# Optimization experiments

Measured on AMD Instinct MI355X. Metric: run time of the kernel, lower is better.

Reference implementation:

```python
import jax, jax.numpy as jnp
import numpy as np

N = 50000
E = 800000
IN, HID, OUT = 20, 64, 2
HEADS, HD = 4, 64
EPS = 1e-5


def setup_inputs() -> dict:
    key = jax.random.key(0)
    ks = jax.random.split(key, 24)
    rn = lambda k, shape, s=0.1: (jax.random.normal(k, shape, dtype=jnp.float32) * s)
    inp = {}
    inp['x'] = jax.random.normal(ks[0], (N, IN), dtype=jnp.float32)
    inp['edge_index'] = jax.random.randint(ks[1], (2, E), 0, N, dtype=jnp.int64)
    # SAGEConv1: lin_l (aggregated msgs, bias), lin_r (root, no bias)
    inp['Wl1'] = rn(ks[2], (IN, HID)); inp['Wr1'] = rn(ks[3], (IN, HID)); inp['b1'] = jnp.zeros((HID,), jnp.float32)
    inp['g1'] = jnp.ones((HID,), jnp.float32); inp['bt1'] = jnp.zeros((HID,), jnp.float32)
    # GATConv: W2 projects to heads*dim; att vectors per head; bias size HID (concat=False)
    inp['W2'] = rn(ks[4], (HID, HEADS * HD)); inp['att_src'] = rn(ks[5], (HEADS, HD)); inp['att_dst'] = rn(ks[6], (HEADS, HD)); inp['b2'] = jnp.zeros((HID,), jnp.float32)
    inp['g2'] = jnp.ones((HID,), jnp.float32); inp['bt2'] = jnp.zeros((HID,), jnp.float32)
    # SAGEConv3: hidden -> hidden//2
    inp['Wl3'] = rn(ks[7], (HID, HID // 2)); inp['Wr3'] = rn(ks[8], (HID, HID // 2)); inp['b3'] = jnp.zeros((HID // 2,), jnp.float32)
    inp['g3'] = jnp.ones((HID // 2,), jnp.float32); inp['bt3'] = jnp.zeros((HID // 2,), jnp.float32)
    # skip + classifier
    inp['Wskip'] = rn(ks[9], (IN, HID // 2)); inp['bskip'] = jnp.zeros((HID // 2,), jnp.float32)
    inp['Wc1'] = rn(ks[10], (HID // 2, 32)); inp['bc1'] = jnp.zeros((32,), jnp.float32)
    inp['Wc2'] = rn(ks[11], (32, OUT)); inp['bc2'] = jnp.zeros((OUT,), jnp.float32)
    return inp


def _bn_eval(h, g, b):
    # eval-mode BatchNorm with freshly initialized running stats (mean=0, var=1)
    return h * (g / jnp.sqrt(1.0 + EPS)) + b


def reference(x, edge_index, Wl1, Wr1, b1, g1, bt1, W2, att_src, att_dst, b2, g2, bt2,
              Wl3, Wr3, b3, g3, bt3, Wskip, bskip, Wc1, bc1, Wc2, bc2):
    src, dst = edge_index[0], edge_index[1]
    deg = jnp.clip(jax.ops.segment_sum(jnp.ones((E,), x.dtype), dst, num_segments=N), 1.0)

    def sage(h, Wl, Wr, b):
        agg = jax.ops.segment_sum(h[src], dst, num_segments=N) / deg[:, None]  # mean aggregation
        return agg @ Wl + h @ Wr + b

    def gat(h):
        hp = (h @ W2).reshape(N, HEADS, HD)                    # [N,H,D]
        a_s = jnp.einsum('nhd,hd->nh', hp, att_src)            # [N,H]
        a_d = jnp.einsum('nhd,hd->nh', hp, att_dst)
        e = jax.nn.leaky_relu(a_s[src] + a_d[dst], 0.2)        # [E,H]
        m = jax.ops.segment_max(e, dst, num_segments=N)        # segment softmax over incoming edges
        ex = jnp.exp(e - m[dst])
        denom = jax.ops.segment_sum(ex, dst, num_segments=N)
        alpha = ex / (denom[dst] + 1e-16)                      # [E,H]
        out = jax.ops.segment_sum(hp[src] * alpha[:, :, None], dst, num_segments=N)  # [N,H,D]
        return out.mean(axis=1) + b2                            # concat=False -> mean over heads

    identity = x @ Wskip + bskip
    h = jax.nn.relu(_bn_eval(sage(x, Wl1, Wr1, b1), g1, bt1))   # dropout inactive (eval)
    h = jax.nn.relu(_bn_eval(gat(h), g2, bt2))
    h = jax.nn.relu(_bn_eval(sage(h, Wl3, Wr3, b3), g3, bt3))
    h = h + identity
    logits = jax.nn.relu(h @ Wc1 + bc1) @ Wc2 + bc2
    return jax.nn.log_softmax(logits, axis=1)
```

## Files before the change

### kernel.cpp

```cpp
#include <hip/hip_runtime.h>
#include <hip/hip_fp16.h>
#include <math.h>

#define NN 50000
#define NE 800000
#define IN_F 20
#define HID 64
#define HEADS 4
#define HD 64
#define CH 32
#define C1 32
#define OUTC 2

__global__ void k_zero_i(int* __restrict__ p, int n){
  int i = blockIdx.x * 256 + threadIdx.x;
  if (i < n) p[i] = 0;
}

__global__ void k_count(const int* __restrict__ dst, int* __restrict__ count){
  int e = blockIdx.x * 256 + threadIdx.x;
  if (e < NE) atomicAdd(&count[dst[e]], 1);
}

__global__ void k_scan_block(const int* __restrict__ in, int* __restrict__ out,
                             int* __restrict__ bsum, int n){
  __shared__ int tmp[256];
  int g = blockIdx.x * 256 + threadIdx.x;
  int v = (g < n) ? in[g] : 0;
  tmp[threadIdx.x] = v;
  __syncthreads();
  for (int o = 1; o < 256; o <<= 1) {
    int t = ((int)threadIdx.x >= o) ? tmp[threadIdx.x - o] : 0;
    __syncthreads();
    tmp[threadIdx.x] += t;
    __syncthreads();
  }
  if (g < n) out[g] = tmp[threadIdx.x] - v;
  if (bsum && threadIdx.x == 255) bsum[blockIdx.x] = tmp[255];
}

__global__ void k_add_off(int* __restrict__ rowptr, const int* __restrict__ bsum_ex, int n){
  int g = blockIdx.x * 256 + threadIdx.x;
  if (g < n) rowptr[g] += bsum_ex[g >> 8];
  if (g == 0) rowptr[NN] = NE;
}

__global__ void k_scatter(const int* __restrict__ src, const int* __restrict__ dst,
                          const int* __restrict__ rowptr, int* __restrict__ cnt2,
                          int* __restrict__ col, int* __restrict__ rowid){
  int e = blockIdx.x * 256 + threadIdx.x;
  if (e >= NE) return;
  int d = dst[e];
  int p = rowptr[d] + atomicAdd(&cnt2[d], 1);
  col[p] = src[e];
  rowid[p] = d;
}

__global__ void k_xhalf(const float* __restrict__ x, __half* __restrict__ xh){
  int i = blockIdx.x * 256 + threadIdx.x;
  if (i < NN * IN_F) xh[i] = __float2half(x[i]);
}

__global__ void k_was(const float* __restrict__ W2, const float* __restrict__ att_src,
                      const float* __restrict__ att_dst,
                      float* __restrict__ was, float* __restrict__ wad){
  int t = threadIdx.x;
  int h = t >> 6, k = t & 63;
  float s = 0.f, dd = 0.f;
  for (int d = 0; d < 64; d++) {
    float w = W2[k * 256 + h * 64 + d];
    s  += w * att_src[h * 64 + d];
    dd += w * att_dst[h * 64 + d];
  }
  was[t] = s; wad[t] = dd;
}

__global__ void k_w2r(const float* __restrict__ W2, float* __restrict__ W2r){
  int i = blockIdx.x * 256 + threadIdx.x;
  if (i >= 256 * 64) return;
  int hk = i >> 6, d = i & 63;
  int h = hk >> 6, k = hk & 63;
  W2r[i] = W2[k * 256 + h * 64 + d];
}

__global__ void k_aggx_gather(const int* __restrict__ rowptr, const int* __restrict__ col,
                              const __half* __restrict__ xh, float* __restrict__ aggx){
  int idx = blockIdx.x * 256 + threadIdx.x;
  int n = idx >> 5, k = idx & 31;
  if (n >= NN || k >= IN_F) return;
  int r0 = rowptr[n], r1 = rowptr[n + 1];
  float acc = 0.f;
  int j = r0;
  for (; j + 4 <= r1; j += 4) {
    int s0 = col[j], s1 = col[j+1], s2 = col[j+2], s3 = col[j+3];
    float v0 = __half2float(xh[s0 * IN_F + k]);
    float v1 = __half2float(xh[s1 * IN_F + k]);
    float v2 = __half2float(xh[s2 * IN_F + k]);
    float v3 = __half2float(xh[s3 * IN_F + k]);
    acc += (v0 + v1) + (v2 + v3);
  }
  for (; j < r1; j++) acc += __half2float(xh[col[j] * IN_F + k]);
  aggx[n * IN_F + k] = acc;
}

__global__ void k_sage1(const float* __restrict__ x, const float* __restrict__ aggx,
                        const int* __restrict__ count,
                        const float* __restrict__ Wl, const float* __restrict__ Wr,
                        const float* __restrict__ b, const float* __restrict__ g,
                        const float* __restrict__ bt,
                        const float* __restrict__ was, const float* __restrict__ wad,
                        __half* __restrict__ h1h, float* __restrict__ a_s,
                        float* __restrict__ a_d){
  __shared__ float sWl[IN_F * HID], sWr[IN_F * HID], sWas[256], sWad[256];
  for (int i = threadIdx.x; i < IN_F * HID; i += 256) { sWl[i] = Wl[i]; sWr[i] = Wr[i]; }
  { int i = threadIdx.x; sWas[i] = was[i]; sWad[i] = wad[i]; }
  __syncthreads();
  int idx = blockIdx.x * 256 + threadIdx.x;
  if (idx >= NN * HID) return;
  int n = idx >> 6, j = idx & 63;
  float inv = 1.f / fmaxf((float)count[n], 1.f);
  const float* xr = x + n * IN_F;
  const float* ar = aggx + n * IN_F;
  float acc = b[j];
  #pragma unroll
  for (int k = 0; k < IN_F; k++)
    acc += (ar[k] * inv) * sWl[k * HID + j] + xr[k] * sWr[k * HID + j];
  acc = acc * (g[j] * rsqrtf(1.f + 1e-5f)) + bt[j];
  acc = fmaxf(acc, 0.f);
  h1h[idx] = __float2half(acc);
  #pragma unroll
  for (int h = 0; h < HEADS; h++) {
    float vs = acc * sWas[h * 64 + j];
    float vd = acc * sWad[h * 64 + j];
    #pragma unroll
    for (int o = 32; o > 0; o >>= 1) { vs += __shfl_down(vs, o); vd += __shfl_down(vd, o); }
    if (j == 0) { a_s[n * 4 + h] = vs; a_d[n * 4 + h] = vd; }
  }
}

__global__ void k_edgep(const int* __restrict__ col, const int* __restrict__ rowid,
                        const float4* __restrict__ a_s4, const float4* __restrict__ a_d4,
                        float4* __restrict__ pe4){
  int j = blockIdx.x * 256 + threadIdx.x;
  if (j >= NE) return;
  float4 as = a_s4[col[j]];
  float4 ad = a_d4[rowid[j]];
  float e0 = as.x + ad.x; e0 = e0 >= 0.f ? e0 : 0.2f * e0;
  float e1 = as.y + ad.y; e1 = e1 >= 0.f ? e1 : 0.2f * e1;
  float e2 = as.z + ad.z; e2 = e2 >= 0.f ? e2 : 0.2f * e2;
  float e3 = as.w + ad.w; e3 = e3 >= 0.f ? e3 : 0.2f * e3;
  pe4[j] = make_float4(__expf(e0), __expf(e1), __expf(e2), __expf(e3));
}

__global__ void k_gat_fused(const int* __restrict__ rowptr, const int* __restrict__ col,
                            const float4* __restrict__ pe4,
                            const __half* __restrict__ h1h, __half* __restrict__ z){
  int wid = threadIdx.x >> 6;
  int lane = threadIdx.x & 63;
  int n = blockIdx.x * 4 + wid;
  if (n >= NN) return;
  int r0 = rowptr[n], r1 = rowptr[n + 1];
  float l0 = 0.f, l1 = 0.f, l2 = 0.f, l3 = 0.f;
  float ac0 = 0.f, ac1 = 0.f, ac2 = 0.f, ac3 = 0.f;
  int j = r0;
  for (; j + 4 <= r1; j += 4) {
    int s0 = col[j], s1 = col[j+1], s2 = col[j+2], s3 = col[j+3];
    float4 p0 = pe4[j], p1 = pe4[j+1], p2 = pe4[j+2], p3 = pe4[j+3];
    float v0 = __half2float(h1h[(size_t)s0 * 64 + lane]);
    float v1 = __half2float(h1h[(size_t)s1 * 64 + lane]);
    float v2 = __half2float(h1h[(size_t)s2 * 64 + lane]);
    float v3 = __half2float(h1h[(size_t)s3 * 64 + lane]);
    l0 += (p0.x + p1.x) + (p2.x + p3.x);
    l1 += (p0.y + p1.y) + (p2.y + p3.y);
    l2 += (p0.z + p1.z) + (p2.z + p3.z);
    l3 += (p0.w + p1.w) + (p2.w + p3.w);
    ac0 += p0.x * v0 + p1.x * v1 + p2.x * v2 + p3.x * v3;
    ac1 += p0.y * v0 + p1.y * v1 + p2.y * v2 + p3.y * v3;
    ac2 += p0.z * v0 + p1.z * v1 + p2.z * v2 + p3.z * v3;
    ac3 += p0.w * v0 + p1.w * v1 + p2.w * v2 + p3.w * v3;
  }
  for (; j < r1; j++) {
    int s = col[j];
    float4 p = pe4[j];
    float v = __half2float(h1h[(size_t)s * 64 + lane]);
    l0 += p.x; l1 += p.y; l2 += p.z; l3 += p.w;
    ac0 += p.x * v; ac1 += p.y * v; ac2 += p.z * v; ac3 += p.w * v;
  }
  __half* zr = z + (size_t)n * 256;
  zr[lane]       = __float2half(ac0 / (4.f * (l0 + 1e-16f)));
  zr[64 + lane]  = __float2half(ac1 / (4.f * (l1 + 1e-16f)));
  zr[128 + lane] = __float2half(ac2 / (4.f * (l2 + 1e-16f)));
  zr[192 + lane] = __float2half(ac3 / (4.f * (l3 + 1e-16f)));
}

__global__ void __launch_bounds__(256) k_zproj(const __half* __restrict__ z,
                      const float* __restrict__ W2r, const float* __restrict__ b2,
                      const float* __restrict__ g2, const float* __restrict__ bt2,
                      float* __restrict__ h2, __half* __restrict__ h2h){
  __shared__ float sz[4][256];
  __shared__ float sacc[4][4][64];
  int tid = threadIdx.x;
  int w = tid >> 6, d = tid & 63;
  float wreg[64];
  #pragma unroll
  for (int i = 0; i < 64; i++) wreg[i] = W2r[(w * 64 + i) * 64 + d];
  float gd = g2[d] * rsqrtf(1.f + 1e-5f), btd = bt2[d], bd = b2[d];
  int n0base = blockIdx.x * 64;
  for (int r = 0; r < 16; r++) {
    int n0 = n0base + r * 4;
    for (int i = tid; i < 512; i += 256) {
      int m = i >> 7, c = (i & 127) * 2;
      int n = n0 + m;
      if (n < NN) {
        __half2 hv = *(const __half2*)(z + (size_t)n * 256 + c);
        float2 f = __half22float2(hv);
        sz[m][c] = f.x; sz[m][c + 1] = f.y;
      } else { sz[m][c] = 0.f; sz[m][c + 1] = 0.f; }
    }
    __syncthreads();
    #pragma unroll
    for (int m = 0; m < 4; m++) {
      float acc = 0.f;
      #pragma unroll
      for (int i = 0; i < 64; i++) acc += sz[m][w * 64 + i] * wreg[i];
      sacc[m][w][d] = acc;
    }
    __syncthreads();
    int n = n0 + w;
    if (n < NN) {
      float rr = sacc[w][0][d] + sacc[w][1][d] + sacc[w][2][d] + sacc[w][3][d] + bd;
      rr = rr * gd + btd;
      rr = fmaxf(rr, 0.f);
      h2[(size_t)n * 64 + d] = rr;
      h2h[(size_t)n * 64 + d] = __float2half(rr);
    }
    __syncthreads();
  }
}

__global__ void k_agg3_gather(const int* __restrict__ rowptr, const int* __restrict__ col,
                              const __half* __restrict__ h2h, float* __restrict__ agg3){
  int idx = blockIdx.x * 256 + threadIdx.x;
  int n = idx >> 6, d = idx & 63;
  if (n >= NN) return;
  int r0 = rowptr[n], r1 = rowptr[n + 1];
  float acc = 0.f;
  int j = r0;
  for (; j + 4 <= r1; j += 4) {
    int s0 = col[j], s1 = col[j+1], s2 = col[j+2], s3 = col[j+3];
    float v0 = __half2float(h2h[(size_t)s0 * 64 + d]);
    float v1 = __half2float(h2h[(size_t)s1 * 64 + d]);
    float v2 = __half2float(h2h[(size_t)s2 * 64 + d]);
    float v3 = __half2float(h2h[(size_t)s3 * 64 + d]);
    acc += (v0 + v1) + (v2 + v3);
  }
  for (; j < r1; j++) acc += __half2float(h2h[(size_t)col[j] * 64 + d]);
  agg3[idx] = acc;
}

__global__ void k_sage3(const float* __restrict__ x, const float* __restrict__ h2,
                        const float* __restrict__ agg3, const int* __restrict__ count,
                        const float* __restrict__ Wl3, const float* __restrict__ Wr3,
                        const float* __restrict__ b3, const float* __restrict__ g3,
                        const float* __restrict__ bt3, const float* __restrict__ Wskip,
                        const float* __restrict__ bskip, float* __restrict__ h3){
  __shared__ float sWl[HID * CH], sWr[HID * CH], sWs[IN_F * CH];
  for (int i = threadIdx.x; i < HID * CH; i += 256) { sWl[i] = Wl3[i]; sWr[i] = Wr3[i]; }
  for (int i = threadIdx.x; i < IN_F * CH; i += 256) sWs[i] = Wskip[i];
  __syncthreads();
  int idx = blockIdx.x * 256 + threadIdx.x;
  if (idx >= NN * CH) return;
  int n = idx >> 5, j = idx & 31;
  float inv = 1.f / fmaxf((float)count[n], 1.f);
  float acc = b3[j];
  const float* ar = agg3 + n * HID;
  const float* hr = h2 + n * HID;
  #pragma unroll
  for (int k = 0; k < HID; k++)
    acc += (ar[k] * inv) * sWl[k * CH + j] + hr[k] * sWr[k * CH + j];
  acc = acc * (g3[j] * rsqrtf(1.f + 1e-5f)) + bt3[j];
  acc = fmaxf(acc, 0.f);
  float idn = bskip[j];
  const float* xr = x + n * IN_F;
  #pragma unroll
  for (int k = 0; k < IN_F; k++) idn += xr[k] * sWs[k * CH + j];
  h3[idx] = acc + idn;
}

__global__ void k_cls(const float* __restrict__ h3, const float* __restrict__ Wc1,
                      const float* __restrict__ bc1, const float* __restrict__ Wc2,
                      const float* __restrict__ bc2, float* __restrict__ out){
  __shared__ float sW1[C1 * C1], sW2[C1 * OUTC], sb1[C1], sb2[OUTC];
  for (int i = threadIdx.x; i < C1 * C1; i += 256) sW1[i] = Wc1[i];
  if (threadIdx.x < C1 * OUTC) sW2[threadIdx.x] = Wc2[threadIdx.x];
  if (threadIdx.x < C1) sb1[threadIdx.x] = bc1[threadIdx.x];
  if (threadIdx.x < OUTC) sb2[threadIdx.x] = bc2[threadIdx.x];
  __syncthreads();
  int n = blockIdx.x * 256 + threadIdx.x;
  if (n >= NN) return;
  float hrow[CH];
  #pragma unroll
  for (int j = 0; j < CH; j++) hrow[j] = h3[n * CH + j];
  float l0 = sb2[0], l1 = sb2[1];
  #pragma unroll
  for (int i = 0; i < C1; i++) {
    float c = sb1[i];
    #pragma unroll
    for (int j = 0; j < CH; j++) c += hrow[j] * sW1[j * C1 + i];
    c = fmaxf(c, 0.f);
    l0 += c * sW2[i * OUTC + 0];
    l1 += c * sW2[i * OUTC + 1];
  }
  float mx = fmaxf(l0, l1);
  float lse = mx + logf(expf(l0 - mx) + expf(l1 - mx));
  out[n * OUTC + 0] = l0 - lse;
  out[n * OUTC + 1] = l1 - lse;
}

extern "C" void kernel_launch(void* const* d_in, const int* in_sizes, int n_in,
                              void* d_out, int out_size, void* d_ws, size_t ws_size,
                              hipStream_t stream) {
  const float* x       = (const float*)d_in[0];
  const int*   ei      = (const int*)d_in[1];
  const float* Wl1     = (const float*)d_in[2];
  const float* Wr1     = (const float*)d_in[3];
  const float* b1      = (const float*)d_in[4];
  const float* g1      = (const float*)d_in[5];
  const float* bt1     = (const float*)d_in[6];
  const float* W2      = (const float*)d_in[7];
  const float* att_src = (const float*)d_in[8];
  const float* att_dst = (const float*)d_in[9];
  const float* b2      = (const float*)d_in[10];
  const float* g2      = (const float*)d_in[11];
  const float* bt2     = (const float*)d_in[12];
  const float* Wl3     = (const float*)d_in[13];
  const float* Wr3     = (const float*)d_in[14];
  const float* b3      = (const float*)d_in[15];
  const float* g3      = (const float*)d_in[16];
  const float* bt3     = (const float*)d_in[17];
  const float* Wskip   = (const float*)d_in[18];
  const float* bskip   = (const float*)d_in[19];
  const float* Wc1     = (const float*)d_in[20];
  const float* bc1     = (const float*)d_in[21];
  const float* Wc2     = (const float*)d_in[22];
  const float* bc2     = (const float*)d_in[23];
  float* out = (float*)d_out;

  const int* src = ei;
  const int* dst = ei + NE;

  float* ws = (float*)d_ws;
  size_t off = 0;
  auto alloc = [&](size_t nf) { size_t o = off; off += (nf + 63) & ~(size_t)63; return o; };
  size_t o_count = alloc(NN);
  size_t o_cnt2  = alloc(NN);
  size_t zero_elems = off;
  size_t o_rowptr = alloc(NN + 1);
  size_t o_bsum   = alloc(256);
  size_t o_bsumex = alloc(256);
  size_t o_col    = alloc(NE);
  size_t o_rowid  = alloc(NE);
  size_t o_pe     = alloc((size_t)NE * 4);
  size_t o_xh     = alloc((size_t)NN * IN_F / 2 + 64);
  size_t o_aggx   = alloc((size_t)NN * IN_F);
  size_t o_h1h    = alloc((size_t)NN * HID / 2 + 64);
  size_t o_as     = alloc((size_t)NN * HEADS);
  size_t o_ad     = alloc((size_t)NN * HEADS);
  size_t o_was    = alloc(256);
  size_t o_wad    = alloc(256);
  size_t o_w2r    = alloc(256 * 64);
  size_t o_z      = alloc((size_t)NN * 256 / 2 + 64);
  size_t o_h2     = alloc((size_t)NN * HID);
  size_t o_h2h    = alloc((size_t)NN * HID / 2 + 64);
  size_t o_agg3   = alloc((size_t)NN * HID);
  size_t o_h3     = alloc((size_t)NN * CH);
  (void)ws_size; (void)in_sizes; (void)n_in; (void)out_size;

  int* count    = (int*)(ws + o_count);
  int* cnt2     = (int*)(ws + o_cnt2);
  int* rowptr   = (int*)(ws + o_rowptr);
  int* bsum     = (int*)(ws + o_bsum);
  int* bsumex   = (int*)(ws + o_bsumex);
  int* col      = (int*)(ws + o_col);
  int* rowid    = (int*)(ws + o_rowid);
  float* pe     = ws + o_pe;
  __half* xh    = (__half*)(ws + o_xh);
  float* aggx   = ws + o_aggx;
  __half* h1h   = (__half*)(ws + o_h1h);
  float* a_s    = ws + o_as;
  float* a_d    = ws + o_ad;
  float* was    = ws + o_was;
  float* wad    = ws + o_wad;
  float* W2r    = ws + o_w2r;
  __half* z     = (__half*)(ws + o_z);
  float* h2     = ws + o_h2;
  __half* h2h   = (__half*)(ws + o_h2h);
  float* agg3   = ws + o_agg3;
  float* h3     = ws + o_h3;

  auto nb = [](long long n) { return (int)((n + 255) / 256); };
  const int nscan = nb(NN);

  k_zero_i<<<nb((long long)zero_elems), 256, 0, stream>>>((int*)ws, (int)zero_elems);
  k_count<<<nb(NE), 256, 0, stream>>>(dst, count);
  k_scan_block<<<nscan, 256, 0, stream>>>(count, rowptr, bsum, NN);
  k_scan_block<<<1, 256, 0, stream>>>(bsum, bsumex, nullptr, nscan);
  k_add_off<<<nscan, 256, 0, stream>>>(rowptr, bsumex, NN);
  k_scatter<<<nb(NE), 256, 0, stream>>>(src, dst, rowptr, cnt2, col, rowid);
  k_xhalf<<<nb((long long)NN * IN_F), 256, 0, stream>>>(x, xh);
  k_was<<<1, 256, 0, stream>>>(W2, att_src, att_dst, was, wad);
  k_w2r<<<64, 256, 0, stream>>>(W2, W2r);
  k_aggx_gather<<<nb((long long)NN * 32), 256, 0, stream>>>(rowptr, col, xh, aggx);
  k_sage1<<<nb((long long)NN * HID), 256, 0, stream>>>(x, aggx, count, Wl1, Wr1, b1, g1, bt1,
                                                       was, wad, h1h, a_s, a_d);
  k_edgep<<<nb(NE), 256, 0, stream>>>(col, rowid, (const float4*)a_s, (const float4*)a_d,
                                      (float4*)pe);
  k_gat_fused<<<nb((long long)NN * 64), 256, 0, stream>>>(rowptr, col, (const float4*)pe, h1h, z);
  k_zproj<<<(NN + 63) / 64, 256, 0, stream>>>(z, W2r, b2, g2, bt2, h2, h2h);
  k_agg3_gather<<<nb((long long)NN * 64), 256, 0, stream>>>(rowptr, col, h2h, agg3);
  k_sage3<<<nb((long long)NN * CH), 256, 0, stream>>>(x, h2, agg3, count, Wl3, Wr3, b3, g3, bt3,
                                                      Wskip, bskip, h3);
  k_cls<<<nb(NN), 256, 0, stream>>>(h3, Wc1, bc1, Wc2, bc2, out);
}
```

Measured before the change: 352.4 us.

## Fuse SAGE3 gather with projection, pack edge arrays, merge prep kernels

Merges the layer-3 neighbor gather and linear projection into one wave-per-node kernel that uses lane shuffles, so the agg3 buffer is no longer written and re-read. Stores src and dst of each CSR edge as one int2 array, and folds the x-to-half conversion, W2 reorder and attention-weight precompute into a single prep kernel. It also replaces the zeroing kernel with hipMemsetAsync, compacts the aggx thread mapping so no lanes sit idle, and stages h3 through shared memory in the classifier. The int2 packing makes gathers that only need the source index read twice as many bytes.

Result: faster. 342.9 us (-2.7%).

```diff
diff --git a/kernel.cpp b/kernel.cpp
--- a/kernel.cpp
+++ b/kernel.cpp
@@ -11,11 +11,6 @@
 #define CH 32
 #define C1 32
 #define OUTC 2
-
-__global__ void k_zero_i(int* __restrict__ p, int n){
-  int i = blockIdx.x * 256 + threadIdx.x;
-  if (i < n) p[i] = 0;
-}
 
 __global__ void k_count(const int* __restrict__ dst, int* __restrict__ count){
   int e = blockIdx.x * 256 + threadIdx.x;
@@ -47,60 +42,55 @@
 
 __global__ void k_scatter(const int* __restrict__ src, const int* __restrict__ dst,
                           const int* __restrict__ rowptr, int* __restrict__ cnt2,
-                          int* __restrict__ col, int* __restrict__ rowid){
+                          int2* __restrict__ colrow){
   int e = blockIdx.x * 256 + threadIdx.x;
   if (e >= NE) return;
   int d = dst[e];
   int p = rowptr[d] + atomicAdd(&cnt2[d], 1);
-  col[p] = src[e];
-  rowid[p] = d;
-}
-
-__global__ void k_xhalf(const float* __restrict__ x, __half* __restrict__ xh){
+  colrow[p] = make_int2(src[e], d);
+}
+
+__global__ void k_prep(const float* __restrict__ x, const float* __restrict__ W2,
+                       const float* __restrict__ att_src, const float* __restrict__ att_dst,
+                       __half* __restrict__ xh, float* __restrict__ was,
+                       float* __restrict__ wad, float* __restrict__ W2r){
   int i = blockIdx.x * 256 + threadIdx.x;
   if (i < NN * IN_F) xh[i] = __float2half(x[i]);
-}
-
-__global__ void k_was(const float* __restrict__ W2, const float* __restrict__ att_src,
-                      const float* __restrict__ att_dst,
-                      float* __restrict__ was, float* __restrict__ wad){
-  int t = threadIdx.x;
-  int h = t >> 6, k = t & 63;
-  float s = 0.f, dd = 0.f;
-  for (int d = 0; d < 64; d++) {
-    float w = W2[k * 256 + h * 64 + d];
-    s  += w * att_src[h * 64 + d];
-    dd += w * att_dst[h * 64 + d];
-  }
-  was[t] = s; wad[t] = dd;
-}
-
-__global__ void k_w2r(const float* __restrict__ W2, float* __restrict__ W2r){
-  int i = blockIdx.x * 256 + threadIdx.x;
-  if (i >= 256 * 64) return;
-  int hk = i >> 6, d = i & 63;
-  int h = hk >> 6, k = hk & 63;
-  W2r[i] = W2[k * 256 + h * 64 + d];
-}
-
-__global__ void k_aggx_gather(const int* __restrict__ rowptr, const int* __restrict__ col,
+  if (i < 256 * 64) {
+    int hk = i >> 6, d = i & 63;
+    int h = hk >> 6, k = hk & 63;
+    W2r[i] = W2[k * 256 + h * 64 + d];
+  }
+  if (i < 256) {
+    int h = i >> 6, k = i & 63;
+    float s = 0.f, dd = 0.f;
+    for (int d = 0; d < 64; d++) {
+      float w = W2[k * 256 + h * 64 + d];
+      s  += w * att_src[h * 64 + d];
+      dd += w * att_dst[h * 64 + d];
+    }
+    was[i] = s; wad[i] = dd;
+  }
+}
+
+__global__ void k_aggx_gather(const int* __restrict__ rowptr, const int2* __restrict__ colrow,
                               const __half* __restrict__ xh, float* __restrict__ aggx){
   int idx = blockIdx.x * 256 + threadIdx.x;
-  int n = idx >> 5, k = idx & 31;
-  if (n >= NN || k >= IN_F) return;
+  if (idx >= NN * IN_F) return;
+  int n = idx / IN_F, k = idx - n * IN_F;
   int r0 = rowptr[n], r1 = rowptr[n + 1];
   float acc = 0.f;
   int j = r0;
   for (; j + 4 <= r1; j += 4) {
-    int s0 = col[j], s1 = col[j+1], s2 = col[j+2], s3 = col[j+3];
+    int s0 = colrow[j].x, s1 = colrow[j+1].x, s2 = colrow[j+2].x, s3 = colrow[j+3].x;
     float v0 = __half2float(xh[s0 * IN_F + k]);
     float v1 = __half2float(xh[s1 * IN_F + k]);
     float v2 = __half2float(xh[s2 * IN_F + k]);
     float v3 = __half2float(xh[s3 * IN_F + k]);
     acc += (v0 + v1) + (v2 + v3);
   }
-  for (; j < r1; j++) acc += __half2float(xh[col[j] * IN_F + k]);
-  aggx[n * IN_F + k] = acc;
+  for (; j < r1; j++) acc += __half2float(xh[colrow[j].x * IN_F + k]);
+  aggx[idx] = acc;
 }
 
 __global__ void k_sage1(const float* __restrict__ x, const float* __restrict__ aggx,
@@ -138,13 +128,14 @@
   }
 }
 
-__global__ void k_edgep(const int* __restrict__ col, const int* __restrict__ rowid,
+__global__ void k_edgep(const int2* __restrict__ colrow,
                         const float4* __restrict__ a_s4, const float4* __restrict__ a_d4,
                         float4* __restrict__ pe4){
   int j = blockIdx.x * 256 + threadIdx.x;
   if (j >= NE) return;
-  float4 as = a_s4[col[j]];
-  float4 ad = a_d4[rowid[j]];
+  int2 cr = colrow[j];
+  float4 as = a_s4[cr.x];
+  float4 ad = a_d4[cr.y];
   float e0 = as.x + ad.x; e0 = e0 >= 0.f ? e0 : 0.2f * e0;
   float e1 = as.y + ad.y; e1 = e1 >= 0.f ? e1 : 0.2f * e1;
   float e2 = as.z + ad.z; e2 = e2 >= 0.f ? e2 : 0.2f * e2;
@@ -152,7 +143,7 @@
   pe4[j] = make_float4(__expf(e0), __expf(e1), __expf(e2), __expf(e3));
 }
 
-__global__ void k_gat_fused(const int* __restrict__ rowptr, const int* __restrict__ col,
+__global__ void k_gat_fused(const int* __restrict__ rowptr, const int2* __restrict__ colrow,
                             const float4* __restrict__ pe4,
                             const __half* __restrict__ h1h, __half* __restrict__ z){
   int wid = threadIdx.x >> 6;
@@ -164,7 +155,7 @@
   float ac0 = 0.f, ac1 = 0.f, ac2 = 0.f, ac3 = 0.f;
   int j = r0;
   for (; j + 4 <= r1; j += 4) {
-    int s0 = col[j], s1 = col[j+1], s2 = col[j+2], s3 = col[j+3];
+    int s0 = colrow[j].x, s1 = colrow[j+1].x, s2 = colrow[j+2].x, s3 = colrow[j+3].x;
     float4 p0 = pe4[j], p1 = pe4[j+1], p2 = pe4[j+2], p3 = pe4[j+3];
     float v0 = __half2float(h1h[(size_t)s0 * 64 + lane]);
     float v1 = __half2float(h1h[(size_t)s1 * 64 + lane]);
@@ -180,7 +171,7 @@
     ac3 += p0.w * v0 + p1.w * v1 + p2.w * v2 + p3.w * v3;
   }
   for (; j < r1; j++) {
-    int s = col[j];
+    int s = colrow[j].x;
     float4 p = pe4[j];
     float v = __half2float(h1h[(size_t)s * 64 + lane]);
     l0 += p.x; l1 += p.y; l2 += p.z; l3 += p.w;
@@ -238,76 +229,90 @@
   }
 }
 
-__global__ void k_agg3_gather(const int* __restrict__ rowptr, const int* __restrict__ col,
-                              const __half* __restrict__ h2h, float* __restrict__ agg3){
-  int idx = blockIdx.x * 256 + threadIdx.x;
-  int n = idx >> 6, d = idx & 63;
-  if (n >= NN) return;
-  int r0 = rowptr[n], r1 = rowptr[n + 1];
-  float acc = 0.f;
-  int j = r0;
-  for (; j + 4 <= r1; j += 4) {
-    int s0 = col[j], s1 = col[j+1], s2 = col[j+2], s3 = col[j+3];
-    float v0 = __half2float(h2h[(size_t)s0 * 64 + d]);
-    float v1 = __half2float(h2h[(size_t)s1 * 64 + d]);
-    float v2 = __half2float(h2h[(size_t)s2 * 64 + d]);
-    float v3 = __half2float(h2h[(size_t)s3 * 64 + d]);
-    acc += (v0 + v1) + (v2 + v3);
-  }
-  for (; j < r1; j++) acc += __half2float(h2h[(size_t)col[j] * 64 + d]);
-  agg3[idx] = acc;
-}
-
-__global__ void k_sage3(const float* __restrict__ x, const float* __restrict__ h2,
-                        const float* __restrict__ agg3, const int* __restrict__ count,
-                        const float* __restrict__ Wl3, const float* __restrict__ Wr3,
-                        const float* __restrict__ b3, const float* __restrict__ g3,
-                        const float* __restrict__ bt3, const float* __restrict__ Wskip,
-                        const float* __restrict__ bskip, float* __restrict__ h3){
+__global__ void __launch_bounds__(256) k_sage3f(
+    const int* __restrict__ rowptr, const int2* __restrict__ colrow,
+    const float* __restrict__ x, const float* __restrict__ h2,
+    const __half* __restrict__ h2h, const int* __restrict__ count,
+    const float* __restrict__ Wl3, const float* __restrict__ Wr3,
+    const float* __restrict__ b3, const float* __restrict__ g3,
+    const float* __restrict__ bt3, const float* __restrict__ Wskip,
+    const float* __restrict__ bskip, float* __restrict__ h3){
   __shared__ float sWl[HID * CH], sWr[HID * CH], sWs[IN_F * CH];
   for (int i = threadIdx.x; i < HID * CH; i += 256) { sWl[i] = Wl3[i]; sWr[i] = Wr3[i]; }
   for (int i = threadIdx.x; i < IN_F * CH; i += 256) sWs[i] = Wskip[i];
   __syncthreads();
-  int idx = blockIdx.x * 256 + threadIdx.x;
-  if (idx >= NN * CH) return;
-  int n = idx >> 5, j = idx & 31;
-  float inv = 1.f / fmaxf((float)count[n], 1.f);
-  float acc = b3[j];
-  const float* ar = agg3 + n * HID;
-  const float* hr = h2 + n * HID;
-  #pragma unroll
-  for (int k = 0; k < HID; k++)
-    acc += (ar[k] * inv) * sWl[k * CH + j] + hr[k] * sWr[k * CH + j];
-  acc = acc * (g3[j] * rsqrtf(1.f + 1e-5f)) + bt3[j];
-  acc = fmaxf(acc, 0.f);
-  float idn = bskip[j];
-  const float* xr = x + n * IN_F;
-  #pragma unroll
-  for (int k = 0; k < IN_F; k++) idn += xr[k] * sWs[k * CH + j];
-  h3[idx] = acc + idn;
-}
-
-__global__ void k_cls(const float* __restrict__ h3, const float* __restrict__ Wc1,
-                      const float* __restrict__ bc1, const float* __restrict__ Wc2,
-                      const float* __restrict__ bc2, float* __restrict__ out){
+  int wid = threadIdx.x >> 6, lane = threadIdx.x & 63;
+  int n = blockIdx.x * 4 + wid;
+  int nc = n < NN ? n : NN - 1;
+  int r0 = rowptr[nc], r1 = rowptr[nc + 1];
+  float aval = 0.f;
+  int j = r0;
+  for (; j + 4 <= r1; j += 4) {
+    int s0 = colrow[j].x, s1 = colrow[j+1].x, s2 = colrow[j+2].x, s3 = colrow[j+3].x;
+    float v0 = __half2float(h2h[(size_t)s0 * 64 + lane]);
+    float v1 = __half2float(h2h[(size_t)s1 * 64 + lane]);
+    float v2 = __half2float(h2h[(size_t)s2 * 64 + lane]);
+    float v3 = __half2float(h2h[(size_t)s3 * 64 + lane]);
+    aval += (v0 + v1) + (v2 + v3);
+  }
+  for (; j < r1; j++) aval += __half2float(h2h[(size_t)colrow[j].x * 64 + lane]);
+  float inv = 1.f / fmaxf((float)count[nc], 1.f);
+  aval *= inv;
+  float hval = h2[(size_t)nc * 64 + lane];
+  int jj = lane & 31;
+  int kbase = (lane >> 5) * 32;
+  float c = 0.f;
+  #pragma unroll
+  for (int k0 = 0; k0 < 32; k0++) {
+    int k = kbase + k0;
+    c += __shfl(aval, k) * sWl[k * CH + jj] + __shfl(hval, k) * sWr[k * CH + jj];
+  }
+  c += __shfl_xor(c, 32);
+  if (lane < 32 && n < NN) {
+    float acc = c + b3[jj];
+    acc = acc * (g3[jj] * rsqrtf(1.f + 1e-5f)) + bt3[jj];
+    acc = fmaxf(acc, 0.f);
+    float idn = bskip[jj];
+    const float* xr = x + (size_t)n * IN_F;
+    #pragma unroll
+    for (int k = 0; k < IN_F; k++) idn += xr[k] * sWs[k * CH + jj];
+    h3[(size_t)n * CH + jj] = acc + idn;
+  }
+}
+
+__global__ void __launch_bounds__(64) k_cls(const float* __restrict__ h3,
+                      const float* __restrict__ Wc1, const float* __restrict__ bc1,
+                      const float* __restrict__ Wc2, const float* __restrict__ bc2,
+                      float* __restrict__ out){
   __shared__ float sW1[C1 * C1], sW2[C1 * OUTC], sb1[C1], sb2[OUTC];
-  for (int i = threadIdx.x; i < C1 * C1; i += 256) sW1[i] = Wc1[i];
-  if (threadIdx.x < C1 * OUTC) sW2[threadIdx.x] = Wc2[threadIdx.x];
-  if (threadIdx.x < C1) sb1[threadIdx.x] = bc1[threadIdx.x];
-  if (threadIdx.x < OUTC) sb2[threadIdx.x] = bc2[threadIdx.x];
+  __shared__ float sh3[64][CH + 1];
+  int tid = threadIdx.x;
+  int n0 = blockIdx.x * 64;
+  for (int i = tid; i < C1 * C1; i += 64) sW1[i] = Wc1[i];
+  if (tid < C1 * OUTC) sW2[tid] = Wc2[tid];
+  if (tid < C1) sb1[tid] = bc1[tid];
+  if (tid < OUTC) sb2[tid] = bc2[tid];
+  for (int i = tid; i < 64 * CH; i += 64) {
+    int m = i >> 5, c = i & 31;
+    int n = n0 + m;
+    sh3[m][c] = (n < NN) ? h3[(size_t)n * CH + c] : 0.f;
+  }
   __syncthreads();
-  int n = blockIdx.x * 256 + threadIdx.x;
+  int n = n0 + tid;
   if (n >= NN) return;
   float hrow[CH];
   #pragma unroll
-  for (int j = 0; j < CH; j++) hrow[j] = h3[n * CH + j];
+  for (int j = 0; j < CH; j++) hrow[j] = sh3[tid][j];
   float l0 = sb2[0], l1 = sb2[1];
   #pragma unroll
   for (int i = 0; i < C1; i++) {
-    float c = sb1[i];
+    float c0 = sb1[i], c1 = 0.f;
     #pragma unroll
-    for (int j = 0; j < CH; j++) c += hrow[j] * sW1[j * C1 + i];
-    c = fmaxf(c, 0.f);
+    for (int j = 0; j < CH; j += 2) {
+      c0 += hrow[j] * sW1[j * C1 + i];
+      c1 += hrow[j + 1] * sW1[(j + 1) * C1 + i];
+    }
+    float c = fmaxf(c0 + c1, 0.f);
     l0 += c * sW2[i * OUTC + 0];
     l1 += c * sW2[i * OUTC + 1];
   }
@@ -358,8 +363,7 @@
   size_t o_rowptr = alloc(NN + 1);
   size_t o_bsum   = alloc(256);
   size_t o_bsumex = alloc(256);
-  size_t o_col    = alloc(NE);
-  size_t o_rowid  = alloc(NE);
+  size_t o_colrow = alloc((size_t)NE * 2);
   size_t o_pe     = alloc((size_t)NE * 4);
   size_t o_xh     = alloc((size_t)NN * IN_F / 2 + 64);
   size_t o_aggx   = alloc((size_t)NN * IN_F);
@@ -372,7 +376,6 @@
   size_t o_z      = alloc((size_t)NN * 256 / 2 + 64);
   size_t o_h2     = alloc((size_t)NN * HID);
   size_t o_h2h    = alloc((size_t)NN * HID / 2 + 64);
-  size_t o_agg3   = alloc((size_t)NN * HID);
   size_t o_h3     = alloc((size_t)NN * CH);
   (void)ws_size; (void)in_sizes; (void)n_in; (void)out_size;
 
@@ -381,8 +384,7 @@
   int* rowptr   = (int*)(ws + o_rowptr);
   int* bsum     = (int*)(ws + o_bsum);
   int* bsumex   = (int*)(ws + o_bsumex);
-  int* col      = (int*)(ws + o_col);
-  int* rowid    = (int*)(ws + o_rowid);
+  int2* colrow  = (int2*)(ws + o_colrow);
   float* pe     = ws + o_pe;
   __half* xh    = (__half*)(ws + o_xh);
   float* aggx   = ws + o_aggx;
@@ -395,30 +397,25 @@
   __half* z     = (__half*)(ws + o_z);
   float* h2     = ws + o_h2;
   __half* h2h   = (__half*)(ws + o_h2h);
-  float* agg3   = ws + o_agg3;
   float* h3     = ws + o_h3;
 
   auto nb = [](long long n) { return (int)((n + 255) / 256); };
   const int nscan = nb(NN);
 
-  k_zero_i<<<nb((long long)zero_elems), 256, 0, stream>>>((int*)ws, (int)zero_elems);
+  hipMemsetAsync(ws, 0, zero_elems * sizeof(int), stream);
   k_count<<<nb(NE), 256, 0, stream>>>(dst, count);
   k_scan_block<<<nscan, 256, 0, stream>>>(count, rowptr, bsum, NN);
   k_scan_block<<<1, 256, 0, stream>>>(bsum, bsumex, nullptr, nscan);
   k_add_off<<<nscan, 256, 0, stream>>>(rowptr, bsumex, NN);
-  k_scatter<<<nb(NE), 256, 0, stream>>>(src, dst, rowptr, cnt2, col, rowid);
-  k_xhalf<<<nb((long long)NN * IN_F), 256, 0, stream>>>(x, xh);
-  k_was<<<1, 256, 0, stream>>>(W2, att_src, att_dst, was, wad);
-  k_w2r<<<64, 256, 0, stream>>>(W2, W2r);
-  k_aggx_gather<<<nb((long long)NN * 32), 256, 0, stream>>>(rowptr, col, xh, aggx);
+  k_scatter<<<nb(NE), 256, 0, stream>>>(src, dst, rowptr, cnt2, colrow);
+  k_prep<<<nb((long long)NN * IN_F), 256, 0, stream>>>(x, W2, att_src, att_dst, xh, was, wad, W2r);
+  k_aggx_gather<<<nb((long long)NN * IN_F), 256, 0, stream>>>(rowptr, colrow, xh, aggx);
   k_sage1<<<nb((long long)NN * HID), 256, 0, stream>>>(x, aggx, count, Wl1, Wr1, b1, g1, bt1,
                                                        was, wad, h1h, a_s, a_d);
-  k_edgep<<<nb(NE), 256, 0, stream>>>(col, rowid, (const float4*)a_s, (const float4*)a_d,
-                                      (float4*)pe);
-  k_gat_fused<<<nb((long long)NN * 64), 256, 0, stream>>>(rowptr, col, (const float4*)pe, h1h, z);
+  k_edgep<<<nb(NE), 256, 0, stream>>>(colrow, (const float4*)a_s, (const float4*)a_d, (float4*)pe);
+  k_gat_fused<<<nb((long long)NN * 64), 256, 0, stream>>>(rowptr, colrow, (const float4*)pe, h1h, z);
   k_zproj<<<(NN + 63) / 64, 256, 0, stream>>>(z, W2r, b2, g2, bt2, h2, h2h);
-  k_agg3_gather<<<nb((long long)NN * 64), 256, 0, stream>>>(rowptr, col, h2h, agg3);
-  k_sage3<<<nb((long long)NN * CH), 256, 0, stream>>>(x, h2, agg3, count, Wl3, Wr3, b3, g3, bt3,
-                                                      Wskip, bskip, h3);
-  k_cls<<<nb(NN), 256, 0, stream>>>(h3, Wc1, bc1, Wc2, bc2, out);
-}
+  k_sage3f<<<(NN + 3) / 4, 256, 0, stream>>>(rowptr, colrow, x, h2, h2h, count,
+                                             Wl3, Wr3, b3, g3, bt3, Wskip, bskip, h3);
+  k_cls<<<(NN + 63) / 64, 64, 0, stream>>>(h3, Wc1, bc1, Wc2, bc2, out);
+}
```
